# Kernel optimization log

Measured on AMD Instinct MI355X. Metric: run time of the kernel, lower is better.

The kernel has to match this reference:

```python
import jax, jax.numpy as jnp
import numpy as np

SOFTENING = 1e-6
EPS = 1e-9
CUTOFF = 0.1
K_NEG = 4
MARGIN = 1.0
KE_FACTOR = 1e-3


def setup_inputs() -> dict:
    key = jax.random.key(0)
    ks = jax.random.split(key, 16)
    B, S, D8, W = 4, 2048, 8, 16
    N = B * S
    return {
        "positions_2d": jax.random.normal(ks[0], (B, S, 2), dtype=jnp.float32),
        "masses": jax.random.uniform(ks[1], (B, S, 1), dtype=jnp.float32),
        "vel_2d": jax.random.normal(ks[2], (N, 2), dtype=jnp.float32),
        "pos_8d": jax.random.normal(ks[3], (N, D8), dtype=jnp.float32),
        "pos_pos_2d": jax.random.normal(ks[4], (N, 2), dtype=jnp.float32),
        "pos_pos_8d": jax.random.normal(ks[5], (N, D8), dtype=jnp.float32),
        "positive_masses": jax.random.uniform(ks[6], (N, 1), dtype=jnp.float32),
        "neg_pos_2d": jax.random.normal(ks[7], (N * K_NEG, 2), dtype=jnp.float32),
        "neg_pos_8d": jax.random.normal(ks[8], (N * K_NEG, D8), dtype=jnp.float32),
        "neg_masses": jax.random.uniform(ks[9], (N * K_NEG, 1), dtype=jnp.float32),
        "exp_masses": jax.random.uniform(ks[10], (N * K_NEG, 1), dtype=jnp.float32),
        "G": jnp.float32(1.0),
        "repulsion_strength": jnp.float32(0.5),
        "well_centers": jax.random.normal(ks[11], (W, D8), dtype=jnp.float32),
        "well_strength": jnp.float32(0.1),
        "temperature": jnp.float32(1.0),
        "entropy_coeff": jnp.float32(0.01),
    }


def _calculate_forces(positions_2d, masses, G, repulsion_strength):
    # positions_2d: [B,S,2], masses: [B,S,1]
    B, S, _ = positions_2d.shape
    # diff[b,i,j] = pos[b,j] - pos[b,i]  -> [B,S,S,2]
    diff = positions_2d[:, None, :, :] - positions_2d[:, :, None, :]
    dist_sq = jnp.sum(diff * diff, axis=-1) + SOFTENING  # [B,S,S]
    dist = jnp.sqrt(dist_sq)
    diag = jnp.eye(S, dtype=bool)  # [S,S], broadcasts over B
    dist_safe = jnp.where(diag, 1.0, dist)
    dist_sq_safe = jnp.where(diag, 1.0, dist_sq)
    mm = masses[:, :, None, 0] * masses[:, None, :, 0]  # [B,S,S]
    attractive = jax.nn.relu(G) * mm / dist_sq_safe
    rep_strength = jax.nn.relu(repulsion_strength)
    repulsive = rep_strength * jax.nn.relu(1.0 - dist_safe / CUTOFF) / (dist_sq_safe * dist_safe + EPS)
    total_mag = repulsive - attractive  # [B,S,S]
    force_vectors = total_mag[..., None] * diff / (dist_safe[..., None] + EPS)
    return jnp.sum(force_vectors, axis=2)  # [B,S,2]


def _cdist(a, b):
    # Euclidean cdist: [N,D] x [W,D] -> [N,W]; W=16 so dense is cheap
    d = a[:, None, :] - b[None, :, :]
    return jnp.sqrt(jnp.sum(d * d, axis=-1))


def _grand_unifying_loss(pos_2d, vel_2d, pos_8d, masses_flat, pos_pos_2d, pos_pos_8d,
                         positive_masses, neg_pos_2d, neg_pos_8d, neg_masses, exp_masses,
                         G, well_centers, well_strength, temperature, entropy_coeff):
    Gp = jax.nn.relu(G)
    dist_pos_2d = jnp.linalg.norm(pos_2d - pos_pos_2d, axis=-1) + EPS  # [N]
    pe_pairwise_pos = -Gp * (masses_flat * positive_masses)[:, 0] / dist_pos_2d
    pos_2d_rep = jnp.repeat(pos_2d, K_NEG, axis=0)  # [N*K,2]
    dist_neg_2d = jnp.linalg.norm(pos_2d_rep - neg_pos_2d, axis=-1) + EPS
    pe_pairwise_neg = -Gp * (exp_masses * neg_masses)[:, 0] / dist_neg_2d

    ws = jax.nn.relu(well_strength)
    all_pos_8d = jnp.concatenate([pos_8d, pos_pos_8d], axis=0)  # [2N,8]
    min_dist_pos = jnp.min(_cdist(all_pos_8d, well_centers), axis=1)
    pe_well_pos = ws * min_dist_pos ** 2
    all_neg_8d = jnp.concatenate([jnp.repeat(pos_8d, K_NEG, axis=0), neg_pos_8d], axis=0)
    min_dist_neg = jnp.min(_cdist(all_neg_8d, well_centers), axis=1)
    pe_well_neg = ws * min_dist_neg ** 2

    U_pos = jnp.mean(pe_pairwise_pos) + jnp.mean(pe_well_pos)
    U_neg = jnp.mean(pe_pairwise_neg) + jnp.mean(pe_well_neg)
    batch_variance = jnp.mean(jnp.var(all_pos_8d, axis=0, ddof=1))  # torch.var is unbiased
    entropy_term = jax.nn.relu(temperature) * jax.nn.relu(entropy_coeff) * batch_variance
    F_pos = U_pos - entropy_term
    F_neg = U_neg - entropy_term
    free_energy_loss = jax.nn.relu(MARGIN + F_pos - F_neg)
    # Original: mean(masses[N,1] * ke[N]) broadcasts to an [N,N] outer product;
    # mean of the outer product == mean(m) * mean(ke) (same value and gradients)
    ke = jnp.sum(vel_2d * vel_2d, axis=-1)  # [N]
    ke_loss = KE_FACTOR * 0.5 * jnp.mean(masses_flat) * jnp.mean(ke)
    return free_energy_loss + ke_loss


def reference(positions_2d, masses, vel_2d, pos_8d, pos_pos_2d, pos_pos_8d,
              positive_masses, neg_pos_2d, neg_pos_8d, neg_masses, exp_masses,
              G, repulsion_strength, well_centers, well_strength, temperature, entropy_coeff):
    forces = _calculate_forces(positions_2d, masses, G, repulsion_strength)
    pos_flat = positions_2d.reshape(-1, 2)
    masses_flat = masses.reshape(-1, 1)
    loss = _grand_unifying_loss(pos_flat, vel_2d, pos_8d, masses_flat, pos_pos_2d,
                                pos_pos_8d, positive_masses, neg_pos_2d, neg_pos_8d,
                                neg_masses, exp_masses, G, well_centers, well_strength,
                                temperature, entropy_coeff)
    return forces, loss
```

## Files before the change

kernel.cpp:

```cpp
#include <hip/hip_runtime.h>

#define N_PTS 8192
#define SEQ   2048
#define BATCH 4
#define KNEG  4
#define NK    32768
#define N2    16384
#define NACC  22

__device__ __forceinline__ float frcp(float x)  { return __builtin_amdgcn_rcpf(x); }
__device__ __forceinline__ float fsqrt_(float x){ return __builtin_amdgcn_sqrtf(x); }

__global__ __launch_bounds__(256) void forces_kernel(
    const float* __restrict__ pos, const float* __restrict__ mass,
    const float* __restrict__ Gptr, const float* __restrict__ Rptr,
    float* __restrict__ out)
{
    const int tid = threadIdx.x;
    const int jc  = blockIdx.x;
    const int it  = blockIdx.y;
    const int b   = blockIdx.z;

    __shared__ float sx[256], sy[256], sm[256];
    const int j0 = jc * 256;
    {
        const int jb = b * SEQ + j0 + tid;
        sx[tid] = pos[jb * 2 + 0];
        sy[tid] = pos[jb * 2 + 1];
        sm[tid] = mass[jb];
    }
    const float Gv = fmaxf(Gptr[0], 0.0f);
    const float Rv = fmaxf(Rptr[0], 0.0f);
    const int   i     = it * 256 + tid;
    const int   ibase = b * SEQ + i;
    const float px = pos[ibase * 2 + 0];
    const float py = pos[ibase * 2 + 1];
    const float ci = Gv * mass[ibase];
    __syncthreads();

    float fx = 0.0f, fy = 0.0f;
    #pragma unroll 4
    for (int j = 0; j < 256; ++j) {
        const float dx = sx[j] - px;
        const float dy = sy[j] - py;
        const float r2 = fmaf(dx, dx, fmaf(dy, dy, 1e-6f));
        const float r  = fsqrt_(r2);
        const float rp = r + 1e-9f;
        float mor = -(ci * sm[j]) * frcp(r2 * rp);
        const float t = fmaf(-10.0f, r, 1.0f);
        if (t > 0.0f) {
            mor += (Rv * t) * frcp(fmaf(r2, r, 1e-9f) * rp);
        }
        fx = fmaf(mor, dx, fx);
        fy = fmaf(mor, dy, fy);
    }
    atomicAdd(&out[ibase * 2 + 0], fx);
    atomicAdd(&out[ibase * 2 + 1], fy);
}

__device__ __forceinline__ float min_dist2(float4 a, float4 b, const float* __restrict__ wc)
{
    float best = 3.4e38f;
    #pragma unroll
    for (int w = 0; w < 16; ++w) {
        const float* c = &wc[w * 8];
        float d, s;
        d = a.x - c[0]; s = d * d;
        d = a.y - c[1]; s = fmaf(d, d, s);
        d = a.z - c[2]; s = fmaf(d, d, s);
        d = a.w - c[3]; s = fmaf(d, d, s);
        d = b.x - c[4]; s = fmaf(d, d, s);
        d = b.y - c[5]; s = fmaf(d, d, s);
        d = b.z - c[6]; s = fmaf(d, d, s);
        d = b.w - c[7]; s = fmaf(d, d, s);
        best = fminf(best, s);
    }
    return best;
}

__global__ __launch_bounds__(256) void loss_partials_kernel(
    const float* __restrict__ pos2,
    const float* __restrict__ mass,
    const float* __restrict__ vel,
    const float* __restrict__ pos8,
    const float* __restrict__ pp2,
    const float* __restrict__ pp8,
    const float* __restrict__ pmass,
    const float* __restrict__ negp2,
    const float* __restrict__ negp8,
    const float* __restrict__ negm,
    const float* __restrict__ expm,
    const float* __restrict__ wellc,
    double* __restrict__ wsacc)
{
    __shared__ float wc[128];
    const int tid = threadIdx.x;
    if (tid < 128) wc[tid] = wellc[tid];
    __syncthreads();

    const int idx = blockIdx.x * 256 + tid;

    double acc[NACC];
    #pragma unroll
    for (int k = 0; k < NACC; ++k) acc[k] = 0.0;

    {
        const float* row = (idx < NK) ? (pos8 + (idx >> 2) * 8)
                                      : (negp8 + (idx - NK) * 8);
        const float4 a = ((const float4*)row)[0];
        const float4 b = ((const float4*)row)[1];
        acc[3] = (double)min_dist2(a, b, wc);
    }
    if (idx < NK) {
        const int i = idx >> 2;
        const float dx = pos2[i * 2 + 0] - negp2[idx * 2 + 0];
        const float dy = pos2[i * 2 + 1] - negp2[idx * 2 + 1];
        const float d  = fsqrt_(fmaf(dx, dx, dy * dy)) + 1e-9f;
        acc[1] = (double)(expm[idx] * negm[idx] / d);
    }
    if (idx < N2) {
        const float* row = (idx < N_PTS) ? (pos8 + idx * 8)
                                         : (pp8 + (idx - N_PTS) * 8);
        const float4 a = ((const float4*)row)[0];
        const float4 b = ((const float4*)row)[1];
        acc[2] = (double)min_dist2(a, b, wc);
        acc[4]  = (double)a.x;  acc[12] = (double)(a.x * a.x);
        acc[5]  = (double)a.y;  acc[13] = (double)(a.y * a.y);
        acc[6]  = (double)a.z;  acc[14] = (double)(a.z * a.z);
        acc[7]  = (double)a.w;  acc[15] = (double)(a.w * a.w);
        acc[8]  = (double)b.x;  acc[16] = (double)(b.x * b.x);
        acc[9]  = (double)b.y;  acc[17] = (double)(b.y * b.y);
        acc[10] = (double)b.z;  acc[18] = (double)(b.z * b.z);
        acc[11] = (double)b.w;  acc[19] = (double)(b.w * b.w);
    }
    if (idx < N_PTS) {
        const float dx = pos2[idx * 2 + 0] - pp2[idx * 2 + 0];
        const float dy = pos2[idx * 2 + 1] - pp2[idx * 2 + 1];
        const float d  = fsqrt_(fmaf(dx, dx, dy * dy)) + 1e-9f;
        acc[0]  = (double)(mass[idx] * pmass[idx] / d);
        acc[20] = (double)mass[idx];
        const float vx = vel[idx * 2 + 0];
        const float vy = vel[idx * 2 + 1];
        acc[21] = (double)fmaf(vx, vx, vy * vy);
    }

    __shared__ double red[4][NACC];
    const int lane = tid & 63, wid = tid >> 6;
    #pragma unroll
    for (int k = 0; k < NACC; ++k) {
        double v = acc[k];
        for (int off = 32; off > 0; off >>= 1) v += __shfl_down(v, off, 64);
        if (lane == 0) red[wid][k] = v;
    }
    __syncthreads();
    if (tid < NACC) {
        const double s = red[0][tid] + red[1][tid] + red[2][tid] + red[3][tid];
        atomicAdd(&wsacc[tid], s);
    }
}

__global__ void finalize_kernel(const double* __restrict__ s,
                                const float* __restrict__ Gptr,
                                const float* __restrict__ wsPtr,
                                const float* __restrict__ tPtr,
                                const float* __restrict__ ecPtr,
                                float* __restrict__ out)
{
    if (threadIdx.x == 0 && blockIdx.x == 0) {
        const double Gp  = fmax((double)Gptr[0], 0.0);
        const double wsp = fmax((double)wsPtr[0], 0.0);
        const double T   = fmax((double)tPtr[0], 0.0);
        const double ec  = fmax((double)ecPtr[0], 0.0);
        const double Nd = 8192.0, NKd = 32768.0, N2d = 16384.0, NK2d = 65536.0;

        const double U_pos = -Gp * s[0] / Nd  + wsp * s[2] / N2d;
        const double U_neg = -Gp * s[1] / NKd + wsp * s[3] / NK2d;

        double var = 0.0;
        for (int d = 0; d < 8; ++d) {
            const double sx = s[4 + d], sxx = s[12 + d];
            var += (sxx - sx * sx / N2d) / (N2d - 1.0);
        }
        var *= 0.125;
        const double ent = T * ec * var;
        const double Fp = U_pos - ent, Fn = U_neg - ent;
        double fel = 1.0 + Fp - Fn;
        if (fel < 0.0) fel = 0.0;
        const double ke_loss = 1e-3 * 0.5 * (s[20] / Nd) * (s[21] / Nd);
        out[16384] = (float)(fel + ke_loss);
    }
}

extern "C" void kernel_launch(void* const* d_in, const int* in_sizes, int n_in,
                              void* d_out, int out_size, void* d_ws, size_t ws_size,
                              hipStream_t stream)
{
    const float* pos   = (const float*)d_in[0];
    const float* mass  = (const float*)d_in[1];
    const float* vel   = (const float*)d_in[2];
    const float* pos8  = (const float*)d_in[3];
    const float* pp2   = (const float*)d_in[4];
    const float* pp8   = (const float*)d_in[5];
    const float* pmass = (const float*)d_in[6];
    const float* negp2 = (const float*)d_in[7];
    const float* negp8 = (const float*)d_in[8];
    const float* negm  = (const float*)d_in[9];
    const float* expm  = (const float*)d_in[10];
    const float* Gp    = (const float*)d_in[11];
    const float* Rp    = (const float*)d_in[12];
    const float* wellc = (const float*)d_in[13];
    const float* wstr  = (const float*)d_in[14];
    const float* temp  = (const float*)d_in[15];
    const float* ecoef = (const float*)d_in[16];

    float*  out = (float*)d_out;
    double* acc = (double*)d_ws;

    hipMemsetAsync(d_out, 0, (size_t)out_size * sizeof(float), stream);
    hipMemsetAsync(d_ws, 0, NACC * sizeof(double), stream);

    forces_kernel<<<dim3(8, 8, 4), 256, 0, stream>>>(pos, mass, Gp, Rp, out);
    loss_partials_kernel<<<256, 256, 0, stream>>>(pos, mass, vel, pos8, pp2, pp8,
                                                  pmass, negp2, negp8, negm, expm,
                                                  wellc, acc);
    finalize_kernel<<<1, 64, 0, stream>>>(acc, Gp, wstr, temp, ecoef, out);
}
```

Before: 122.7 us.

## Fuse forces, loss partials and finalize into one kernel with last-block reduction

```diff
diff --git a/kernel.cpp b/kernel.cpp
--- a/kernel.cpp
+++ b/kernel.cpp
@@ -1,62 +1,16 @@
 #include <hip/hip_runtime.h>
 
-#define N_PTS 8192
-#define SEQ   2048
-#define BATCH 4
-#define KNEG  4
-#define NK    32768
-#define N2    16384
-#define NACC  22
+#define SEQ    2048
+#define N_PTS  8192
+#define NK     32768
+#define N2     16384
+#define NACC   22
+#define NLOSSBLK 256
+#define SLOT_DOUBLES (NLOSSBLK * NACC)
+#define CTR_OFFSET   (SLOT_DOUBLES * 8)
 
 __device__ __forceinline__ float frcp(float x)  { return __builtin_amdgcn_rcpf(x); }
 __device__ __forceinline__ float fsqrt_(float x){ return __builtin_amdgcn_sqrtf(x); }
-
-__global__ __launch_bounds__(256) void forces_kernel(
-    const float* __restrict__ pos, const float* __restrict__ mass,
-    const float* __restrict__ Gptr, const float* __restrict__ Rptr,
-    float* __restrict__ out)
-{
-    const int tid = threadIdx.x;
-    const int jc  = blockIdx.x;
-    const int it  = blockIdx.y;
-    const int b   = blockIdx.z;
-
-    __shared__ float sx[256], sy[256], sm[256];
-    const int j0 = jc * 256;
-    {
-        const int jb = b * SEQ + j0 + tid;
-        sx[tid] = pos[jb * 2 + 0];
-        sy[tid] = pos[jb * 2 + 1];
-        sm[tid] = mass[jb];
-    }
-    const float Gv = fmaxf(Gptr[0], 0.0f);
-    const float Rv = fmaxf(Rptr[0], 0.0f);
-    const int   i     = it * 256 + tid;
-    const int   ibase = b * SEQ + i;
-    const float px = pos[ibase * 2 + 0];
-    const float py = pos[ibase * 2 + 1];
-    const float ci = Gv * mass[ibase];
-    __syncthreads();
-
-    float fx = 0.0f, fy = 0.0f;
-    #pragma unroll 4
-    for (int j = 0; j < 256; ++j) {
-        const float dx = sx[j] - px;
-        const float dy = sy[j] - py;
-        const float r2 = fmaf(dx, dx, fmaf(dy, dy, 1e-6f));
-        const float r  = fsqrt_(r2);
-        const float rp = r + 1e-9f;
-        float mor = -(ci * sm[j]) * frcp(r2 * rp);
-        const float t = fmaf(-10.0f, r, 1.0f);
-        if (t > 0.0f) {
-            mor += (Rv * t) * frcp(fmaf(r2, r, 1e-9f) * rp);
-        }
-        fx = fmaf(mor, dx, fx);
-        fy = fmaf(mor, dy, fy);
-    }
-    atomicAdd(&out[ibase * 2 + 0], fx);
-    atomicAdd(&out[ibase * 2 + 1], fy);
-}
 
 __device__ __forceinline__ float min_dist2(float4 a, float4 b, const float* __restrict__ wc)
 {
@@ -78,8 +32,8 @@
     return best;
 }
 
-__global__ __launch_bounds__(256) void loss_partials_kernel(
-    const float* __restrict__ pos2,
+__global__ __launch_bounds__(256) void fused_kernel(
+    const float* __restrict__ pos,
     const float* __restrict__ mass,
     const float* __restrict__ vel,
     const float* __restrict__ pos8,
@@ -90,15 +44,85 @@
     const float* __restrict__ negp8,
     const float* __restrict__ negm,
     const float* __restrict__ expm,
+    const float* __restrict__ Gptr,
+    const float* __restrict__ Rptr,
     const float* __restrict__ wellc,
-    double* __restrict__ wsacc)
+    const float* __restrict__ wstr,
+    const float* __restrict__ tPtr,
+    const float* __restrict__ ecPtr,
+    float* __restrict__ out,
+    double* __restrict__ slots,
+    unsigned int* __restrict__ ctr)
 {
-    __shared__ float wc[128];
     const int tid = threadIdx.x;
+    const int blk = blockIdx.x;
+
+    if (blk < 256) {
+        __shared__ float sx[SEQ], sy[SEQ], sm[SEQ];
+        __shared__ float rf[2][8][32];
+
+        const int b  = blk >> 6;
+        const int it = blk & 63;
+        const int rowbase = b * SEQ;
+
+        const float2* p2 = (const float2*)pos;
+        for (int k = tid; k < SEQ; k += 256) {
+            const float2 v = p2[rowbase + k];
+            sx[k] = v.x; sy[k] = v.y;
+            sm[k] = mass[rowbase + k];
+        }
+        const float Gv = fmaxf(Gptr[0], 0.0f);
+        const float Rv = fmaxf(Rptr[0], 0.0f);
+        __syncthreads();
+
+        const int il = tid & 31;
+        const int js = tid >> 5;
+        const int iloc = it * 32 + il;
+        const float px = sx[iloc];
+        const float py = sy[iloc];
+        const float ci = Gv * sm[iloc];
+
+        float fx = 0.0f, fy = 0.0f;
+        const int j0 = js * 256;
+        #pragma unroll 4
+        for (int jj = 0; jj < 256; ++jj) {
+            const int j = j0 + jj;
+            const float dx = sx[j] - px;
+            const float dy = sy[j] - py;
+            const float r2 = fmaf(dx, dx, fmaf(dy, dy, 1e-6f));
+            const float r  = fsqrt_(r2);
+            const float rp = r + 1e-9f;
+            float mor = -(ci * sm[j]) * frcp(r2 * rp);
+            const float t = fmaf(-10.0f, r, 1.0f);
+            if (t > 0.0f) {
+                mor += (Rv * t) * frcp(fmaf(r2, r, 1e-9f) * rp);
+            }
+            fx = fmaf(mor, dx, fx);
+            fy = fmaf(mor, dy, fy);
+        }
+        rf[0][js][il] = fx;
+        rf[1][js][il] = fy;
+        __syncthreads();
+        if (tid < 64) {
+            const int comp = tid >> 5, i2 = tid & 31;
+            float s = 0.0f;
+            #pragma unroll
+            for (int q = 0; q < 8; ++q) s += rf[comp][q][i2];
+            out[(rowbase + it * 32 + i2) * 2 + comp] = s;
+        }
+        return;
+    }
+
+    __shared__ float  wc[128];
+    __shared__ double red[4][NACC];
+    __shared__ int    lastflag;
+
     if (tid < 128) wc[tid] = wellc[tid];
-    __syncthreads();
-
-    const int idx = blockIdx.x * 256 + tid;
+    if (tid == 0)  lastflag = 0;
+    __syncthreads();
+
+    const int lb  = blk - 256;
+    const int idx = lb * 256 + tid;
 
     double acc[NACC];
     #pragma unroll
@@ -113,8 +137,8 @@
     }
     if (idx < NK) {
         const int i = idx >> 2;
-        const float dx = pos2[i * 2 + 0] - negp2[idx * 2 + 0];
-        const float dy = pos2[i * 2 + 1] - negp2[idx * 2 + 1];
+        const float dx = pos[i * 2 + 0] - negp2[idx * 2 + 0];
+        const float dy = pos[i * 2 + 1] - negp2[idx * 2 + 1];
         const float d  = fsqrt_(fmaf(dx, dx, dy * dy)) + 1e-9f;
         acc[1] = (double)(expm[idx] * negm[idx] / d);
     }
@@ -134,8 +158,8 @@
         acc[11] = (double)b.w;  acc[19] = (double)(b.w * b.w);
     }
     if (idx < N_PTS) {
-        const float dx = pos2[idx * 2 + 0] - pp2[idx * 2 + 0];
-        const float dy = pos2[idx * 2 + 1] - pp2[idx * 2 + 1];
+        const float dx = pos[idx * 2 + 0] - pp2[idx * 2 + 0];
+        const float dy = pos[idx * 2 + 1] - pp2[idx * 2 + 1];
         const float d  = fsqrt_(fmaf(dx, dx, dy * dy)) + 1e-9f;
         acc[0]  = (double)(mass[idx] * pmass[idx] / d);
         acc[20] = (double)mass[idx];
@@ -144,7 +168,6 @@
         acc[21] = (double)fmaf(vx, vx, vy * vy);
     }
 
-    __shared__ double red[4][NACC];
     const int lane = tid & 63, wid = tid >> 6;
     #pragma unroll
     for (int k = 0; k < NACC; ++k) {
@@ -154,21 +177,33 @@
     }
     __syncthreads();
     if (tid < NACC) {
-        const double s = red[0][tid] + red[1][tid] + red[2][tid] + red[3][tid];
-        atomicAdd(&wsacc[tid], s);
-    }
-}
-
-__global__ void finalize_kernel(const double* __restrict__ s,
-                                const float* __restrict__ Gptr,
-                                const float* __restrict__ wsPtr,
-                                const float* __restrict__ tPtr,
-                                const float* __restrict__ ecPtr,
-                                float* __restrict__ out)
-{
-    if (threadIdx.x == 0 && blockIdx.x == 0) {
+        slots[lb * NACC + tid] = red[0][tid] + red[1][tid] + red[2][tid] + red[3][tid];
+    }
+    __syncthreads();
+    if (tid == 0) {
+        __threadfence();
+        const unsigned int ticket = atomicAdd(ctr, 1u);
+        if (ticket == NLOSSBLK - 1) lastflag = 1;
+    }
+    __syncthreads();
+    if (!lastflag) return;
+
+    __threadfence();
+    #pragma unroll
+    for (int k = 0; k < NACC; ++k) {
+        double v = slots[tid * NACC + k];
+        for (int off = 32; off > 0; off >>= 1) v += __shfl_down(v, off, 64);
+        if (lane == 0) red[wid][k] = v;
+    }
+    __syncthreads();
+    if (tid == 0) {
+        double s[NACC];
+        #pragma unroll
+        for (int k = 0; k < NACC; ++k)
+            s[k] = red[0][k] + red[1][k] + red[2][k] + red[3][k];
+
         const double Gp  = fmax((double)Gptr[0], 0.0);
-        const double wsp = fmax((double)wsPtr[0], 0.0);
+        const double wsp = fmax((double)wstr[0], 0.0);
         const double T   = fmax((double)tPtr[0], 0.0);
         const double ec  = fmax((double)ecPtr[0], 0.0);
         const double Nd = 8192.0, NKd = 32768.0, N2d = 16384.0, NK2d = 65536.0;
@@ -178,8 +213,8 @@
 
         double var = 0.0;
         for (int d = 0; d < 8; ++d) {
-            const double sx = s[4 + d], sxx = s[12 + d];
-            var += (sxx - sx * sx / N2d) / (N2d - 1.0);
+            const double sx_ = s[4 + d], sxx = s[12 + d];
+            var += (sxx - sx_ * sx_ / N2d) / (N2d - 1.0);
         }
         var *= 0.125;
         const double ent = T * ec * var;
@@ -213,15 +248,14 @@
     const float* temp  = (const float*)d_in[15];
     const float* ecoef = (const float*)d_in[16];
 
-    float*  out = (float*)d_out;
-    double* acc = (double*)d_ws;
-
-    hipMemsetAsync(d_out, 0, (size_t)out_size * sizeof(float), stream);
-    hipMemsetAsync(d_ws, 0, NACC * sizeof(double), stream);
-
-    forces_kernel<<<dim3(8, 8, 4), 256, 0, stream>>>(pos, mass, Gp, Rp, out);
-    loss_partials_kernel<<<256, 256, 0, stream>>>(pos, mass, vel, pos8, pp2, pp8,
-                                                  pmass, negp2, negp8, negm, expm,
-                                                  wellc, acc);
-    finalize_kernel<<<1, 64, 0, stream>>>(acc, Gp, wstr, temp, ecoef, out);
+    float*        out   = (float*)d_out;
+    double*       slots = (double*)d_ws;
+    unsigned int* ctr   = (unsigned int*)((char*)d_ws + CTR_OFFSET);
+
+    hipMemsetAsync(ctr, 0, sizeof(unsigned int), stream);
+
+    fused_kernel<<<512, 256, 0, stream>>>(pos, mass, vel, pos8, pp2, pp8, pmass,
+                                          negp2, negp8, negm, expm, Gp, Rp,
+                                          wellc, wstr, temp, ecoef,
+                                          out, slots, ctr);
 }
```

Result: faster. 107.6 us (-12.3%).
